# Optimization experiments

Hardware: AMD Instinct MI355X
Metric: run time of the kernel (lower is better)

The kernel has to match this reference:

```python
import jax, jax.numpy as jnp
import numpy as np

# dims (see shape_source)
B, S, N, F_IN = 8, 32, 512, 24   # batch, sections, nodes/section, node feat
C = 56                            # GAT out_channels (hidden_size)
EB, ES = 262144, 8192             # bend edges (over S*N nodes), section edges (over N nodes)
ED = 4                            # edge_dim
NEG_SLOPE_ATT = 0.2               # GATConv leaky_relu slope


def setup_inputs() -> dict:
    key = jax.random.key(0)
    ks = jax.random.split(key, 24)
    sd = 0.1
    inp = {}
    inp["x"] = jax.random.normal(ks[0], (B, S, N, F_IN), jnp.float32)
    inp["bend_edge_index"] = jax.random.randint(ks[1], (2, EB), 0, S * N)
    inp["section_edge_index"] = jax.random.randint(ks[2], (2, ES), 0, N)
    inp["bend_edge_attr"] = jax.random.normal(ks[3], (B, EB, ED), jnp.float32)
    inp["section_edge_attr"] = jax.random.normal(ks[4], (B, ES, ED), jnp.float32)
    # edge encoder Linear(4, 4)
    inp["enc_W"] = jax.random.normal(ks[5], (ED, ED), jnp.float32) * sd
    inp["enc_b"] = jax.random.normal(ks[6], (ED,), jnp.float32) * sd
    # GAT (bend) params: heads=1, concat=False
    inp["Wb"] = jax.random.normal(ks[7], (F_IN, C), jnp.float32) * sd
    inp["a_src_b"] = jax.random.normal(ks[8], (C,), jnp.float32) * sd
    inp["a_dst_b"] = jax.random.normal(ks[9], (C,), jnp.float32) * sd
    inp["We_b"] = jax.random.normal(ks[10], (ED, C), jnp.float32) * sd
    inp["a_e_b"] = jax.random.normal(ks[11], (C,), jnp.float32) * sd
    inp["bias_b"] = jax.random.normal(ks[12], (C,), jnp.float32) * sd
    # GAT (section) params
    inp["Ws"] = jax.random.normal(ks[13], (F_IN, C), jnp.float32) * sd
    inp["a_src_s"] = jax.random.normal(ks[14], (C,), jnp.float32) * sd
    inp["a_dst_s"] = jax.random.normal(ks[15], (C,), jnp.float32) * sd
    inp["We_s"] = jax.random.normal(ks[16], (ED, C), jnp.float32) * sd
    inp["a_e_s"] = jax.random.normal(ks[17], (C,), jnp.float32) * sd
    inp["bias_s"] = jax.random.normal(ks[18], (C,), jnp.float32) * sd
    # learnable mixing weights (nn.Parameter(torch.ones(2)))
    inp["mix_w"] = jnp.ones((2,), jnp.float32)
    return inp


def _segment_softmax(logits, seg, num_segments):
    m = jax.ops.segment_max(logits, seg, num_segments=num_segments)
    ex = jnp.exp(logits - m[seg])
    s = jax.ops.segment_sum(ex, seg, num_segments=num_segments)
    return ex / (s[seg] + 1e-16)


def _gat(x, edge_index, e_attr, W, a_src, a_dst, We, a_e, bias, num_nodes):
    """PyG GATConv (heads=1, concat=False, edge_dim) in eval mode on one graph."""
    h = x @ W                              # [Nn, C]
    e = e_attr @ We                        # [E, C] (lin_edge has no bias)
    src, dst = edge_index[0], edge_index[1]
    alpha_src = h @ a_src                  # [Nn]
    alpha_dst = h @ a_dst                  # [Nn]
    logits = jax.nn.leaky_relu(alpha_src[src] + alpha_dst[dst] + e @ a_e,
                               NEG_SLOPE_ATT)           # [E]
    att = _segment_softmax(logits, dst, num_nodes)      # softmax over incoming edges
    out = jax.ops.segment_sum(att[:, None] * h[src], dst, num_segments=num_nodes)
    return out + bias


def reference(x, bend_edge_index, section_edge_index, bend_edge_attr,
              section_edge_attr, enc_W, enc_b, Wb, a_src_b, a_dst_b, We_b,
              a_e_b, bias_b, Ws, a_src_s, a_dst_s, We_s, a_e_s, bias_s, mix_w):
    b, s, n, f = x.shape
    enc_bend = bend_edge_attr @ enc_W + enc_b       # [B, EB, ED]
    enc_sec = section_edge_attr @ enc_W + enc_b     # [B, ES, ED]

    # --- bend graph: one big graph of S*N nodes per sample, vmapped over batch
    x_flat = x.reshape(b, s * n, f)
    gat_bend = jax.vmap(lambda xi, ei: _gat(xi, bend_edge_index, ei, Wb,
                                            a_src_b, a_dst_b, We_b, a_e_b,
                                            bias_b, s * n))
    x_b_out = jax.nn.leaky_relu(gat_bend(x_flat, enc_bend), 0.01)  # [B, S*N, C]

    # --- section graphs: N-node graph per (sample, section); edge attrs shared
    # across sections within a sample (per the original loop).
    x_sec = x.reshape(b * s, n, f)
    enc_sec_rep = jnp.broadcast_to(enc_sec[:, None], (b, s) + enc_sec.shape[1:])
    enc_sec_rep = enc_sec_rep.reshape(b * s, enc_sec.shape[1], enc_sec.shape[2])
    gat_sec = jax.vmap(lambda xi, ei: _gat(xi, section_edge_index, ei, Ws,
                                           a_src_s, a_dst_s, We_s, a_e_s,
                                           bias_s, n))
    x_s_out = gat_sec(x_sec, enc_sec_rep).reshape(b, s * n, -1)    # [B, S*N, C]

    w = jax.nn.softmax(mix_w)
    return w[0] * x_b_out + w[1] * x_s_out
```

## Files before the change

### kernel.cpp

```cpp
#include <hip/hip_runtime.h>
#include <hip/hip_fp16.h>
#include <math.h>

#define BB 8
#define SS 32
#define NN 512
#define FIN 24
#define CC 56
#define EBN 262144
#define ESN 8192
#define EDD 4
#define NG (SS*NN)
#define BCAP 128
#define SCAP 128
#define HROW (CC*2)

__device__ __forceinline__ float wave_sum(float v) {
    #pragma unroll
    for (int o = 32; o > 0; o >>= 1) v += __shfl_xor(v, o);
    return v;
}

__global__ void k0_init(const float* enc_W, const float* enc_b,
                        const float* Wb, const float* a_src_b, const float* a_dst_b,
                        const float* We_b, const float* a_e_b,
                        const float* Ws, const float* a_src_s, const float* a_dst_s,
                        const float* We_s, const float* a_e_s,
                        const float* mix_w, float* P, int* cnts) {
    int i = blockIdx.x * blockDim.x + threadIdx.x;
    if (i < NG + NN) cnts[i] = 0;
    if (blockIdx.x == 0) {
        int t = threadIdx.x;
        if (t < 96) {
            int v = t / FIN, f = t % FIN;
            const float* W = (v < 2) ? Wb : Ws;
            const float* a = (v == 0) ? a_src_b : (v == 1) ? a_dst_b
                           : (v == 2) ? a_src_s : a_dst_s;
            float d = 0.f;
            for (int c = 0; c < CC; ++c) d = fmaf(W[f*CC + c], a[c], d);
            P[16 + t] = d;
        }
        if (t == 0) {
            float tb[EDD], ts[EDD];
            for (int j = 0; j < EDD; ++j) {
                float vb = 0.f, vs = 0.f;
                for (int c = 0; c < CC; ++c) {
                    vb += We_b[j*CC + c] * a_e_b[c];
                    vs += We_s[j*CC + c] * a_e_s[c];
                }
                tb[j] = vb; ts[j] = vs;
            }
            float cb = 0.f, cs = 0.f;
            for (int j = 0; j < EDD; ++j) { cb += enc_b[j]*tb[j]; cs += enc_b[j]*ts[j]; }
            for (int d = 0; d < EDD; ++d) {
                float ub = 0.f, us = 0.f;
                for (int j = 0; j < EDD; ++j) {
                    ub += enc_W[d*EDD + j] * tb[j];
                    us += enc_W[d*EDD + j] * ts[j];
                }
                P[d] = ub; P[5 + d] = us;
            }
            P[4] = cb; P[9] = cs;
            float m0 = mix_w[0], m1 = mix_w[1];
            float mm = fmaxf(m0, m1);
            float e0 = expf(m0 - mm), e1 = expf(m1 - mm);
            float inv = 1.f / (e0 + e1);
            P[10] = e0 * inv; P[11] = e1 * inv;
        }
    }
}

#define FNB 64
#define FEAT_NB (BB*NG/FNB)
#define FILLB_NB ((EBN+255)/256)
#define FILLS_NB ((ESN+255)/256)
#define ELOG_NB ((BB*(EBN+ESN)+255)/256)

__global__ __launch_bounds__(256, 4) void k1_all(
        const float* __restrict__ x,
        const int* __restrict__ bend_ei, const int* __restrict__ sec_ei,
        const float* __restrict__ bend_attr, const float* __restrict__ sec_attr,
        const float* __restrict__ Wb, const float* __restrict__ Ws,
        const float* __restrict__ P,
        unsigned short* __restrict__ h_b, unsigned short* __restrict__ h_s,
        float* __restrict__ asb, float* __restrict__ adb,
        float* __restrict__ ass, float* __restrict__ ads,
        float* __restrict__ elog_b, float* __restrict__ elog_s,
        int* __restrict__ bcnt, int2* __restrict__ bbuck,
        int* __restrict__ scnt, int2* __restrict__ sbuck) {
    __shared__ float xs[FNB * FIN];
    int blk = blockIdx.x;
    int t = threadIdx.x;
    if (blk < FEAT_NB) {
        const float4* xg = (const float4*)(x + (size_t)blk * FNB * FIN);
        float4* xs4 = (float4*)xs;
        #pragma unroll
        for (int i = 0; i < (FNB*FIN/4 + 255) / 256; ++i) {
            int idx = t + i * 256;
            if (idx < FNB*FIN/4) xs4[idx] = xg[idx];
        }
        int w = t >> 6, lane = t & 63;
        int nl0 = w * (FNB / 4);
        __syncthreads();
        #pragma unroll 1
        for (int m = 0; m < 2; ++m) {
            const float* W = m ? Ws : Wb;
            unsigned short* h = m ? h_s : h_b;
            float* asx = m ? ass : asb;
            float* adx = m ? ads : adb;
            float wc[FIN];
            #pragma unroll
            for (int f = 0; f < FIN; ++f) {
                float v = 0.f;
                if (lane < CC) v = W[f*CC + lane];
                else if (lane < 58) v = P[16 + m*48 + (lane - 56)*FIN + f];
                wc[f] = v;
            }
            #pragma unroll 2
            for (int n0 = 0; n0 < FNB / 4; ++n0) {
                int nl = nl0 + n0;
                size_t node = (size_t)blk * FNB + nl;
                const float4* xr = (const float4*)(xs + nl * FIN);
                float acc = 0.f;
                #pragma unroll
                for (int q = 0; q < FIN/4; ++q) {
                    float4 v = xr[q];
                    acc = fmaf(v.x, wc[4*q+0], acc);
                    acc = fmaf(v.y, wc[4*q+1], acc);
                    acc = fmaf(v.z, wc[4*q+2], acc);
                    acc = fmaf(v.w, wc[4*q+3], acc);
                }
                if (lane < CC) h[node*CC + lane] = __half_as_ushort(__float2half(acc));
                else if (lane == 56) asx[node] = acc;
                else if (lane == 57) adx[node] = acc;
            }
        }
    } else if (blk < FEAT_NB + FILLB_NB) {
        int i = (blk - FEAT_NB) * 256 + t;
        if (i < EBN) {
            int d = bend_ei[EBN + i];
            int p = atomicAdd(&bcnt[d], 1);
            if (p < BCAP) bbuck[(size_t)d * BCAP + p] = make_int2(bend_ei[i], i);
        }
    } else if (blk < FEAT_NB + FILLB_NB + FILLS_NB) {
        int i = (blk - FEAT_NB - FILLB_NB) * 256 + t;
        if (i < ESN) {
            int d = sec_ei[ESN + i];
            int p = atomicAdd(&scnt[d], 1);
            if (p < SCAP) sbuck[(size_t)d * SCAP + p] = make_int2(sec_ei[i], i);
        }
    } else {
        int i = (blk - FEAT_NB - FILLB_NB - FILLS_NB) * 256 + t;
        const int nb = BB * EBN;
        if (i < nb) {
            float4 a = ((const float4*)bend_attr)[i];
            elog_b[i] = fmaf(a.x, P[0], fmaf(a.y, P[1], fmaf(a.z, P[2], fmaf(a.w, P[3], P[4]))));
        } else if (i < nb + BB * ESN) {
            int j = i - nb;
            float4 a = ((const float4*)sec_attr)[j];
            elog_s[j] = fmaf(a.x, P[5], fmaf(a.y, P[6], fmaf(a.z, P[7], fmaf(a.w, P[8], P[9]))));
        }
    }
}

__device__ __forceinline__ float accum_f16(const unsigned short* pArr,
                                           const unsigned int* oArr,
                                           int deg, const char* __restrict__ hB,
                                           unsigned int cl2,
                                           unsigned int& psum2) {
    float a0 = 0.f, a1 = 0.f;
    const uint4* pv = (const uint4*)pArr;
    const uint4* ov = (const uint4*)oArr;
    int ng8 = (deg + 7) >> 3;
    for (int j = 0; j < ng8; ++j) {
        uint4 pq = pv[j];
        uint4 oa = ov[2*j];
        uint4 ob = ov[2*j+1];
        unsigned int h0 = *(const unsigned short*)(hB + (oa.x + cl2));
        unsigned int h1 = *(const unsigned short*)(hB + (oa.y + cl2));
        unsigned int h2 = *(const unsigned short*)(hB + (oa.z + cl2));
        unsigned int h3 = *(const unsigned short*)(hB + (oa.w + cl2));
        unsigned int h4 = *(const unsigned short*)(hB + (ob.x + cl2));
        unsigned int h5 = *(const unsigned short*)(hB + (ob.y + cl2));
        unsigned int h6 = *(const unsigned short*)(hB + (ob.z + cl2));
        unsigned int h7 = *(const unsigned short*)(hB + (ob.w + cl2));
        asm("v_pk_add_f16 %0, %0, %1" : "+v"(psum2) : "v"(pq.x));
        asm("v_pk_add_f16 %0, %0, %1" : "+v"(psum2) : "v"(pq.y));
        asm("v_pk_add_f16 %0, %0, %1" : "+v"(psum2) : "v"(pq.z));
        asm("v_pk_add_f16 %0, %0, %1" : "+v"(psum2) : "v"(pq.w));
        asm("v_fma_mix_f32 %0, %1, %2, %0 op_sel:[0,0,0] op_sel_hi:[1,1,0]" : "+v"(a0) : "v"(pq.x), "v"(h0));
        asm("v_fma_mix_f32 %0, %1, %2, %0 op_sel:[1,0,0] op_sel_hi:[1,1,0]" : "+v"(a1) : "v"(pq.x), "v"(h1));
        asm("v_fma_mix_f32 %0, %1, %2, %0 op_sel:[0,0,0] op_sel_hi:[1,1,0]" : "+v"(a0) : "v"(pq.y), "v"(h2));
        asm("v_fma_mix_f32 %0, %1, %2, %0 op_sel:[1,0,0] op_sel_hi:[1,1,0]" : "+v"(a1) : "v"(pq.y), "v"(h3));
        asm("v_fma_mix_f32 %0, %1, %2, %0 op_sel:[0,0,0] op_sel_hi:[1,1,0]" : "+v"(a0) : "v"(pq.z), "v"(h4));
        asm("v_fma_mix_f32 %0, %1, %2, %0 op_sel:[1,0,0] op_sel_hi:[1,1,0]" : "+v"(a1) : "v"(pq.z), "v"(h5));
        asm("v_fma_mix_f32 %0, %1, %2, %0 op_sel:[0,0,0] op_sel_hi:[1,1,0]" : "+v"(a0) : "v"(pq.w), "v"(h6));
        asm("v_fma_mix_f32 %0, %1, %2, %0 op_sel:[1,0,0] op_sel_hi:[1,1,0]" : "+v"(a1) : "v"(pq.w), "v"(h7));
    }
    return a0 + a1;
}

__device__ __noinline__ float gat_big(const int2* __restrict__ buck, int deg,
                                      const float* __restrict__ asrc,
                                      const float* __restrict__ el,
                                      const char* __restrict__ hB,
                                      float adg, int lane, unsigned int cl2,
                                      unsigned short* pArr, unsigned int* oArr) {
    if (deg <= 0) return 0.f;
    float acc = 0.f, sum = 0.f;
    for (int k0 = 0; k0 < deg; k0 += 64) {
        int k = k0 + lane;
        bool v = k < deg;
        int2 se = buck[v ? k : 0];
        float lg = asrc[(unsigned)se.x] + adg + el[(unsigned)se.y];
        lg = fmaxf(lg, 0.2f * lg);
        float p = v ? __expf(lg) : 0.f;
        asm volatile("s_waitcnt lgkmcnt(0)" ::: "memory");
        pArr[lane] = __half_as_ushort(__float2half(p));
        oArr[lane] = (unsigned int)(se.x * HROW);
        sum += wave_sum(p);
        asm volatile("s_waitcnt lgkmcnt(0)" ::: "memory");
        int valid = (deg - k0) < 64 ? (deg - k0) : 64;
        unsigned int dummy = 0;
        acc += accum_f16(pArr, oArr, valid, hB, cl2, dummy);
    }
    return acc * __builtin_amdgcn_rcpf(sum + 1e-16f);
}

__global__ __launch_bounds__(256, 8) void k2_gather(
        const int* __restrict__ bcnt, const int2* __restrict__ bbuck,
        const int* __restrict__ scnt, const int2* __restrict__ sbuck,
        const unsigned short* __restrict__ h_b, const unsigned short* __restrict__ h_s,
        const float* __restrict__ asb, const float* __restrict__ adb,
        const float* __restrict__ ass, const float* __restrict__ ads,
        const float* __restrict__ elog_b, const float* __restrict__ elog_s,
        const float* __restrict__ bias_b, const float* __restrict__ bias_s,
        const float* __restrict__ P, float* __restrict__ out) {
    __shared__ __align__(16) unsigned short pLds[4][2][64];
    __shared__ __align__(16) unsigned int   oLds[4][2][64];
    int blk = blockIdx.x;
    int b = blk & 7;
    int w = threadIdx.x >> 6;
    unsigned int g = (((unsigned)blk >> 3) << 2) + w;
    unsigned int lane = threadIdx.x & 63;
    unsigned int cl2 = (lane < CC ? lane : 0) * 2;

    int degb = bcnt[g];  degb = degb < BCAP ? degb : BCAP;
    unsigned int sct = g >> 9;
    unsigned int n = g & (NN - 1);
    int degs = scnt[n];  degs = degs < SCAP ? degs : SCAP;

    const int2* bb = bbuck + (size_t)g * BCAP;
    const int2* sb = sbuck + (size_t)n * SCAP;
    const float* asrcb = asb + (size_t)b * NG;
    const float* elb   = elog_b + (size_t)b * EBN;
    const char* hbB = (const char*)(h_b + (size_t)b * NG * CC);
    size_t basebg = (size_t)b * NG + (size_t)sct * NN;
    const float* asrcs = ass + basebg;
    const float* els   = elog_s + (size_t)b * ESN;
    const char* hsB = (const char*)(h_s + basebg * CC);
    float adgb = adb[(size_t)b * NG + g];
    float adgs = ads[basebg + n];

    float vb, vs;
    if (degb <= 64 && degs <= 64) {
        bool vB = lane < (unsigned)degb, vS = lane < (unsigned)degs;
        int2 seb = bb[vB ? lane : 0u];
        int2 ses = sb[vS ? lane : 0u];
        float lgb = asrcb[(unsigned)seb.x] + adgb + elb[(unsigned)seb.y];
        float lgs = asrcs[(unsigned)ses.x] + adgs + els[(unsigned)ses.y];
        lgb = fmaxf(lgb, 0.2f * lgb);
        lgs = fmaxf(lgs, 0.2f * lgs);
        float pb = vB ? __expf(lgb) : 0.f;
        float ps = vS ? __expf(lgs) : 0.f;
        pLds[w][0][lane] = __half_as_ushort(__float2half(pb));
        pLds[w][1][lane] = __half_as_ushort(__float2half(ps));
        oLds[w][0][lane] = (unsigned int)(seb.x * HROW);
        oLds[w][1][lane] = (unsigned int)(ses.x * HROW);
        asm volatile("s_waitcnt lgkmcnt(0)" ::: "memory");
        unsigned int psumb = 0u, psums = 0u;
        float accb = accum_f16(&pLds[w][0][0], &oLds[w][0][0], degb, hbB, cl2, psumb);
        float accs = accum_f16(&pLds[w][1][0], &oLds[w][1][0], degs, hsB, cl2, psums);
        __half2 hb2 = __builtin_bit_cast(__half2, psumb);
        __half2 hs2 = __builtin_bit_cast(__half2, psums);
        float sumb = __low2float(hb2) + __high2float(hb2);
        float sums = __low2float(hs2) + __high2float(hs2);
        vb = accb * __builtin_amdgcn_rcpf(sumb + 1e-16f);
        vs = accs * __builtin_amdgcn_rcpf(sums + 1e-16f);
    } else {
        vb = gat_big(bb, degb, asrcb, elb, hbB, adgb, lane, cl2,
                     &pLds[w][0][0], &oLds[w][0][0]);
        vs = gat_big(sb, degs, asrcs, els, hsB, adgs, lane, cl2,
                     &pLds[w][1][0], &oLds[w][1][0]);
    }

    if (lane < CC) {
        float ob = vb + bias_b[lane];
        ob = fmaxf(ob, 0.01f * ob);
        float os = vs + bias_s[lane];
        out[((size_t)b * NG + g) * CC + lane] = P[10] * ob + P[11] * os;
    }
}

extern "C" void kernel_launch(void* const* d_in, const int* in_sizes, int n_in,
                              void* d_out, int out_size, void* d_ws, size_t ws_size,
                              hipStream_t stream) {
    const float* x          = (const float*)d_in[0];
    const int*   bend_ei    = (const int*)d_in[1];
    const int*   sec_ei     = (const int*)d_in[2];
    const float* bend_attr  = (const float*)d_in[3];
    const float* sec_attr   = (const float*)d_in[4];
    const float* enc_W      = (const float*)d_in[5];
    const float* enc_b      = (const float*)d_in[6];
    const float* Wb         = (const float*)d_in[7];
    const float* a_src_b    = (const float*)d_in[8];
    const float* a_dst_b    = (const float*)d_in[9];
    const float* We_b       = (const float*)d_in[10];
    const float* a_e_b      = (const float*)d_in[11];
    const float* bias_b     = (const float*)d_in[12];
    const float* Ws         = (const float*)d_in[13];
    const float* a_src_s    = (const float*)d_in[14];
    const float* a_dst_s    = (const float*)d_in[15];
    const float* We_s       = (const float*)d_in[16];
    const float* a_e_s      = (const float*)d_in[17];
    const float* bias_s     = (const float*)d_in[18];
    const float* mix_w      = (const float*)d_in[19];
    float* out = (float*)d_out;

    char* base = (char*)d_ws;
    size_t off = 0;
    auto alloc = [&](size_t bytes) -> char* {
        off = (off + 255) & ~(size_t)255;
        char* p = base + off;
        off += bytes;
        return p;
    };
    float* P       = (float*)alloc(128 * sizeof(float));
    int* bcnt      = (int*)alloc((NG + NN) * sizeof(int));
    int* scnt      = bcnt + NG;
    int2* bbuck    = (int2*)alloc((size_t)NG * BCAP * sizeof(int2));
    int2* sbuck    = (int2*)alloc((size_t)NN * SCAP * sizeof(int2));
    unsigned short* h_b = (unsigned short*)alloc((size_t)BB * NG * CC * sizeof(unsigned short));
    unsigned short* h_s = (unsigned short*)alloc((size_t)BB * NG * CC * sizeof(unsigned short));
    float* asb     = (float*)alloc((size_t)BB * NG * sizeof(float));
    float* adb     = (float*)alloc((size_t)BB * NG * sizeof(float));
    float* ass     = (float*)alloc((size_t)BB * NG * sizeof(float));
    float* ads     = (float*)alloc((size_t)BB * NG * sizeof(float));
    float* elog_b  = (float*)alloc((size_t)BB * EBN * sizeof(float));
    float* elog_s  = (float*)alloc((size_t)BB * ESN * sizeof(float));
    (void)ws_size; (void)in_sizes; (void)n_in; (void)out_size;

    k0_init<<<(NG + NN + 255) / 256, 256, 0, stream>>>(enc_W, enc_b,
                                                       Wb, a_src_b, a_dst_b, We_b, a_e_b,
                                                       Ws, a_src_s, a_dst_s, We_s, a_e_s,
                                                       mix_w, P, bcnt);

    int k1_blocks = FEAT_NB + FILLB_NB + FILLS_NB + ELOG_NB;
    k1_all<<<k1_blocks, 256, 0, stream>>>(x, bend_ei, sec_ei, bend_attr, sec_attr,
                                          Wb, Ws, P, h_b, h_s, asb, adb, ass, ads,
                                          elog_b, elog_s, bcnt, bbuck, scnt, sbuck);

    int k2_blocks = 8 * (NG / 4);
    k2_gather<<<k2_blocks, 256, 0, stream>>>(bcnt, bbuck, scnt, sbuck, h_b, h_s,
                                             asb, adb, ass, ads, elog_b, elog_s,
                                             bias_b, bias_s, P, out);
}
```

Measured before the change: 141.7 us.

## Scatter edge logits into CSR bucket order during edge fill

Edge attention logits are now computed inside the bucket-fill pass and written into the destination-sorted CSR slot for every batch element. The buckets shrink from int2 (source, edge id) pairs to plain source ints. The gather kernel then reads logits contiguously instead of through a random indirect lookup by edge id. In exchange, the fill pass does scattered writes of eight floats per edge into a larger strided buffer of about 8*NG*BCAP floats, and the separate elog blocks are removed.

```diff
diff --git a/kernel.cpp b/kernel.cpp
--- a/kernel.cpp
+++ b/kernel.cpp
@@ -74,7 +74,6 @@
 #define FEAT_NB (BB*NG/FNB)
 #define FILLB_NB ((EBN+255)/256)
 #define FILLS_NB ((ESN+255)/256)
-#define ELOG_NB ((BB*(EBN+ESN)+255)/256)
 
 __global__ __launch_bounds__(256, 4) void k1_all(
         const float* __restrict__ x,
@@ -85,9 +84,8 @@
         unsigned short* __restrict__ h_b, unsigned short* __restrict__ h_s,
         float* __restrict__ asb, float* __restrict__ adb,
         float* __restrict__ ass, float* __restrict__ ads,
-        float* __restrict__ elog_b, float* __restrict__ elog_s,
-        int* __restrict__ bcnt, int2* __restrict__ bbuck,
-        int* __restrict__ scnt, int2* __restrict__ sbuck) {
+        int* __restrict__ bcnt, int* __restrict__ bbuck, float* __restrict__ elb_csr,
+        int* __restrict__ scnt, int* __restrict__ sbuck, float* __restrict__ els_csr) {
     __shared__ float xs[FNB * FIN];
     int blk = blockIdx.x;
     int t = threadIdx.x;
@@ -138,27 +136,36 @@
     } else if (blk < FEAT_NB + FILLB_NB) {
         int i = (blk - FEAT_NB) * 256 + t;
         if (i < EBN) {
+            int s = bend_ei[i];
             int d = bend_ei[EBN + i];
             int p = atomicAdd(&bcnt[d], 1);
-            if (p < BCAP) bbuck[(size_t)d * BCAP + p] = make_int2(bend_ei[i], i);
-        }
-    } else if (blk < FEAT_NB + FILLB_NB + FILLS_NB) {
+            if (p < BCAP) {
+                bbuck[d * BCAP + p] = s;
+                size_t slot = (size_t)d * BCAP + p;
+                #pragma unroll
+                for (int b = 0; b < BB; ++b) {
+                    float4 a = ((const float4*)bend_attr)[(size_t)b * EBN + i];
+                    elb_csr[(size_t)b * (NG * BCAP) + slot] =
+                        fmaf(a.x, P[0], fmaf(a.y, P[1], fmaf(a.z, P[2], fmaf(a.w, P[3], P[4]))));
+                }
+            }
+        }
+    } else {
         int i = (blk - FEAT_NB - FILLB_NB) * 256 + t;
         if (i < ESN) {
+            int s = sec_ei[i];
             int d = sec_ei[ESN + i];
             int p = atomicAdd(&scnt[d], 1);
-            if (p < SCAP) sbuck[(size_t)d * SCAP + p] = make_int2(sec_ei[i], i);
-        }
-    } else {
-        int i = (blk - FEAT_NB - FILLB_NB - FILLS_NB) * 256 + t;
-        const int nb = BB * EBN;
-        if (i < nb) {
-            float4 a = ((const float4*)bend_attr)[i];
-            elog_b[i] = fmaf(a.x, P[0], fmaf(a.y, P[1], fmaf(a.z, P[2], fmaf(a.w, P[3], P[4]))));
-        } else if (i < nb + BB * ESN) {
-            int j = i - nb;
-            float4 a = ((const float4*)sec_attr)[j];
-            elog_s[j] = fmaf(a.x, P[5], fmaf(a.y, P[6], fmaf(a.z, P[7], fmaf(a.w, P[8], P[9]))));
+            if (p < SCAP) {
+                sbuck[d * SCAP + p] = s;
+                size_t slot = (size_t)d * SCAP + p;
+                #pragma unroll
+                for (int b = 0; b < BB; ++b) {
+                    float4 a = ((const float4*)sec_attr)[(size_t)b * ESN + i];
+                    els_csr[(size_t)b * (NN * SCAP) + slot] =
+                        fmaf(a.x, P[5], fmaf(a.y, P[6], fmaf(a.z, P[7], fmaf(a.w, P[8], P[9]))));
+                }
+            }
         }
     }
 }
@@ -200,9 +207,9 @@
     return a0 + a1;
 }
 
-__device__ __noinline__ float gat_big(const int2* __restrict__ buck, int deg,
+__device__ __noinline__ float gat_big(const int* __restrict__ buck,
+                                      const float* __restrict__ elc, int deg,
                                       const float* __restrict__ asrc,
-                                      const float* __restrict__ el,
                                       const char* __restrict__ hB,
                                       float adg, int lane, unsigned int cl2,
                                       unsigned short* pArr, unsigned int* oArr) {
@@ -211,13 +218,14 @@
     for (int k0 = 0; k0 < deg; k0 += 64) {
         int k = k0 + lane;
         bool v = k < deg;
-        int2 se = buck[v ? k : 0];
-        float lg = asrc[(unsigned)se.x] + adg + el[(unsigned)se.y];
+        unsigned idx = v ? (unsigned)k : 0u;
+        unsigned s = (unsigned)buck[idx];
+        float lg = asrc[s] + adg + elc[idx];
         lg = fmaxf(lg, 0.2f * lg);
         float p = v ? __expf(lg) : 0.f;
         asm volatile("s_waitcnt lgkmcnt(0)" ::: "memory");
         pArr[lane] = __half_as_ushort(__float2half(p));
-        oArr[lane] = (unsigned int)(se.x * HROW);
+        oArr[lane] = s * HROW;
         sum += wave_sum(p);
         asm volatile("s_waitcnt lgkmcnt(0)" ::: "memory");
         int valid = (deg - k0) < 64 ? (deg - k0) : 64;
@@ -228,12 +236,13 @@
 }
 
 __global__ __launch_bounds__(256, 8) void k2_gather(
-        const int* __restrict__ bcnt, const int2* __restrict__ bbuck,
-        const int* __restrict__ scnt, const int2* __restrict__ sbuck,
+        const int* __restrict__ bcnt, const int* __restrict__ bbuck,
+        const float* __restrict__ elb_csr,
+        const int* __restrict__ scnt, const int* __restrict__ sbuck,
+        const float* __restrict__ els_csr,
         const unsigned short* __restrict__ h_b, const unsigned short* __restrict__ h_s,
         const float* __restrict__ asb, const float* __restrict__ adb,
         const float* __restrict__ ass, const float* __restrict__ ads,
-        const float* __restrict__ elog_b, const float* __restrict__ elog_s,
         const float* __restrict__ bias_b, const float* __restrict__ bias_s,
         const float* __restrict__ P, float* __restrict__ out) {
     __shared__ __align__(16) unsigned short pLds[4][2][64];
@@ -250,14 +259,14 @@
     unsigned int n = g & (NN - 1);
     int degs = scnt[n];  degs = degs < SCAP ? degs : SCAP;
 
-    const int2* bb = bbuck + (size_t)g * BCAP;
-    const int2* sb = sbuck + (size_t)n * SCAP;
+    const int* bb = bbuck + (size_t)g * BCAP;
+    const float* elbp = elb_csr + (size_t)b * (NG * BCAP) + (size_t)g * BCAP;
+    const int* sb = sbuck + (size_t)n * SCAP;
+    const float* elsp = els_csr + (size_t)b * (NN * SCAP) + (size_t)n * SCAP;
     const float* asrcb = asb + (size_t)b * NG;
-    const float* elb   = elog_b + (size_t)b * EBN;
     const char* hbB = (const char*)(h_b + (size_t)b * NG * CC);
     size_t basebg = (size_t)b * NG + (size_t)sct * NN;
     const float* asrcs = ass + basebg;
-    const float* els   = elog_s + (size_t)b * ESN;
     const char* hsB = (const char*)(h_s + basebg * CC);
     float adgb = adb[(size_t)b * NG + g];
     float adgs = ads[basebg + n];
@@ -265,18 +274,22 @@
     float vb, vs;
     if (degb <= 64 && degs <= 64) {
         bool vB = lane < (unsigned)degb, vS = lane < (unsigned)degs;
-        int2 seb = bb[vB ? lane : 0u];
-        int2 ses = sb[vS ? lane : 0u];
-        float lgb = asrcb[(unsigned)seb.x] + adgb + elb[(unsigned)seb.y];
-        float lgs = asrcs[(unsigned)ses.x] + adgs + els[(unsigned)ses.y];
+        unsigned slb = vB ? lane : 0u;
+        unsigned sls = vS ? lane : 0u;
+        unsigned srcb = (unsigned)bb[slb];
+        unsigned srcs = (unsigned)sb[sls];
+        float elbv = elbp[slb];
+        float elsv = elsp[sls];
+        float lgb = asrcb[srcb] + adgb + elbv;
+        float lgs = asrcs[srcs] + adgs + elsv;
         lgb = fmaxf(lgb, 0.2f * lgb);
         lgs = fmaxf(lgs, 0.2f * lgs);
         float pb = vB ? __expf(lgb) : 0.f;
         float ps = vS ? __expf(lgs) : 0.f;
         pLds[w][0][lane] = __half_as_ushort(__float2half(pb));
         pLds[w][1][lane] = __half_as_ushort(__float2half(ps));
-        oLds[w][0][lane] = (unsigned int)(seb.x * HROW);
-        oLds[w][1][lane] = (unsigned int)(ses.x * HROW);
+        oLds[w][0][lane] = srcb * HROW;
+        oLds[w][1][lane] = srcs * HROW;
         asm volatile("s_waitcnt lgkmcnt(0)" ::: "memory");
         unsigned int psumb = 0u, psums = 0u;
         float accb = accum_f16(&pLds[w][0][0], &oLds[w][0][0], degb, hbB, cl2, psumb);
@@ -288,9 +301,9 @@
         vb = accb * __builtin_amdgcn_rcpf(sumb + 1e-16f);
         vs = accs * __builtin_amdgcn_rcpf(sums + 1e-16f);
     } else {
-        vb = gat_big(bb, degb, asrcb, elb, hbB, adgb, lane, cl2,
+        vb = gat_big(bb, elbp, degb, asrcb, hbB, adgb, lane, cl2,
                      &pLds[w][0][0], &oLds[w][0][0]);
-        vs = gat_big(sb, degs, asrcs, els, hsB, adgs, lane, cl2,
+        vs = gat_big(sb, elsp, degs, asrcs, hsB, adgs, lane, cl2,
                      &pLds[w][1][0], &oLds[w][1][0]);
     }
 
@@ -335,19 +348,19 @@
         off += bytes;
         return p;
     };
-    float* P       = (float*)alloc(128 * sizeof(float));
-    int* bcnt      = (int*)alloc((NG + NN) * sizeof(int));
-    int* scnt      = bcnt + NG;
-    int2* bbuck    = (int2*)alloc((size_t)NG * BCAP * sizeof(int2));
-    int2* sbuck    = (int2*)alloc((size_t)NN * SCAP * sizeof(int2));
+    float* P        = (float*)alloc(128 * sizeof(float));
+    int* bcnt       = (int*)alloc((NG + NN) * sizeof(int));
+    int* scnt       = bcnt + NG;
+    int* bbuck      = (int*)alloc((size_t)NG * BCAP * sizeof(int));
+    int* sbuck      = (int*)alloc((size_t)NN * SCAP * sizeof(int));
+    float* elb_csr  = (float*)alloc((size_t)BB * NG * BCAP * sizeof(float));
+    float* els_csr  = (float*)alloc((size_t)BB * NN * SCAP * sizeof(float));
     unsigned short* h_b = (unsigned short*)alloc((size_t)BB * NG * CC * sizeof(unsigned short));
     unsigned short* h_s = (unsigned short*)alloc((size_t)BB * NG * CC * sizeof(unsigned short));
-    float* asb     = (float*)alloc((size_t)BB * NG * sizeof(float));
-    float* adb     = (float*)alloc((size_t)BB * NG * sizeof(float));
-    float* ass     = (float*)alloc((size_t)BB * NG * sizeof(float));
-    float* ads     = (float*)alloc((size_t)BB * NG * sizeof(float));
-    float* elog_b  = (float*)alloc((size_t)BB * EBN * sizeof(float));
-    float* elog_s  = (float*)alloc((size_t)BB * ESN * sizeof(float));
+    float* asb      = (float*)alloc((size_t)BB * NG * sizeof(float));
+    float* adb      = (float*)alloc((size_t)BB * NG * sizeof(float));
+    float* ass      = (float*)alloc((size_t)BB * NG * sizeof(float));
+    float* ads      = (float*)alloc((size_t)BB * NG * sizeof(float));
     (void)ws_size; (void)in_sizes; (void)n_in; (void)out_size;
 
     k0_init<<<(NG + NN + 255) / 256, 256, 0, stream>>>(enc_W, enc_b,
@@ -355,13 +368,13 @@
                                                        Ws, a_src_s, a_dst_s, We_s, a_e_s,
                                                        mix_w, P, bcnt);
 
-    int k1_blocks = FEAT_NB + FILLB_NB + FILLS_NB + ELOG_NB;
+    int k1_blocks = FEAT_NB + FILLB_NB + FILLS_NB;
     k1_all<<<k1_blocks, 256, 0, stream>>>(x, bend_ei, sec_ei, bend_attr, sec_attr,
                                           Wb, Ws, P, h_b, h_s, asb, adb, ass, ads,
-                                          elog_b, elog_s, bcnt, bbuck, scnt, sbuck);
+                                          bcnt, bbuck, elb_csr, scnt, sbuck, els_csr);
 
     int k2_blocks = 8 * (NG / 4);
-    k2_gather<<<k2_blocks, 256, 0, stream>>>(bcnt, bbuck, scnt, sbuck, h_b, h_s,
-                                             asb, adb, ass, ads, elog_b, elog_s,
+    k2_gather<<<k2_blocks, 256, 0, stream>>>(bcnt, bbuck, elb_csr, scnt, sbuck, els_csr,
+                                             h_b, h_s, asb, adb, ass, ads,
                                              bias_b, bias_s, P, out);
 }
```

Result: no change. 139.7 us (-1.4%).
